# Optimization experiments

Hardware: AMD Instinct MI355X
Metric: run time of the kernel (lower is better)

Reference implementation:

```python
import jax, jax.numpy as jnp
import numpy as np

B, C, E = 64, 32, 4
D_MODEL, PRED_LEN = 1024, 720
L_LIST = [32, 16, 8, 4]  # seq_len=512 / patch_sizes [16,32,64,128]
EPS = float(np.finfo(float).eps)


def setup_inputs() -> dict:
    key = jax.random.key(0)
    ks = jax.random.split(key, 16)
    inp = {}
    for i, L in enumerate(L_LIST):
        inp[f"xs{i}"] = jax.random.normal(ks[i], (B, C, L, D_MODEL), dtype=jnp.float32)
    inp["gates"] = jax.random.uniform(ks[4], (B, E), dtype=jnp.float32)
    w_scale = 1.0 / np.sqrt(D_MODEL)
    for i in range(E):
        inp[f"W{i}"] = jax.random.normal(ks[5 + i], (D_MODEL, PRED_LEN), dtype=jnp.float32) * w_scale
        inp[f"b{i}"] = jax.random.normal(ks[9 + i], (PRED_LEN,), dtype=jnp.float32) * 0.01
    return inp


def reference(xs0, xs1, xs2, xs3, gates, W0, b0, W1, b1, W2, b2, W3, b3):
    xs = [xs0, xs1, xs2, xs3]
    Ws = [W0, W1, W2, W3]
    bs = [b0, b1, b2, b3]
    # per-expert linear on last token: [B,C,D] @ [D,P] + [P] -> [B,C,P]
    outs = jnp.stack(
        [jnp.einsum("bcd,dp->bcp", x[:, :, -1, :], W) + b for x, W, b in zip(xs, Ws, bs)]
    )  # [E,B,C,P]
    # dense-gate combine(): sum_e gates[b,e] * exp(out_e[b])
    combined = jnp.einsum("ebcp,be->bcp", jnp.exp(outs), gates)  # [B,C,P]
    combined = jnp.where(combined == 0, EPS, combined)
    out = jnp.log(combined)  # [B,C,P]
    return out.transpose(0, 2, 1)  # 'B C P -> B P C'
```

## Files before the change

### kernel.cpp

```cpp
#include <hip/hip_runtime.h>
#include <hip/hip_bf16.h>


typedef __attribute__((ext_vector_type(4))) float f32x4;
typedef __attribute__((ext_vector_type(8))) short bf16x8;
typedef __attribute__((ext_vector_type(4))) unsigned short u16x4;
typedef __attribute__((ext_vector_type(8))) unsigned short u16x8;

#define EPSV 2.2204460492503131e-16f

__device__ __forceinline__ unsigned short f2bf(float f) {
  unsigned u = __builtin_bit_cast(unsigned, f);
  u += 0x7fffu + ((u >> 16) & 1u);
  return (unsigned short)(u >> 16);
}
__device__ __forceinline__ float bf2f(unsigned short h) {
  unsigned u = ((unsigned)h) << 16;
  return __builtin_bit_cast(float, u);
}

__device__ __forceinline__ void gload_lds16(const void* g, void* l) {
  __builtin_amdgcn_global_load_lds(
      (const __attribute__((address_space(1))) unsigned int*)g,
      (__attribute__((address_space(3))) unsigned int*)l, 16, 0, 0);
}

__global__ __launch_bounds__(256) void prep_fused(
    const float* __restrict__ xs0, const float* __restrict__ xs1,
    const float* __restrict__ xs2, const float* __restrict__ xs3,
    const float* __restrict__ W0, const float* __restrict__ W1,
    const float* __restrict__ W2, const float* __restrict__ W3,
    unsigned short* __restrict__ Xb, unsigned short* __restrict__ Wb)
{
  __shared__ __align__(16) unsigned short tile[64 * 72];
  const int tid = threadIdx.x;
  if (blockIdx.x < 4096) {
    const int i = blockIdx.x * 256 + tid;
    const int e = i >> 18;
    const int rem = i & 262143;
    const int m = rem >> 7;
    const int kc = rem & 127;
    const float* xp = (e == 0) ? xs0 : (e == 1) ? xs1 : (e == 2) ? xs2 : xs3;
    const int L = 32 >> e;
    const float* src = xp + ((size_t)m * L + (L - 1)) * 1024 + kc * 8;
    f32x4 v0 = *(const f32x4*)src;
    f32x4 v1 = *(const f32x4*)(src + 4);
    u16x8 pk;
    pk[0] = f2bf(v0[0]); pk[1] = f2bf(v0[1]); pk[2] = f2bf(v0[2]); pk[3] = f2bf(v0[3]);
    pk[4] = f2bf(v1[0]); pk[5] = f2bf(v1[1]); pk[6] = f2bf(v1[2]); pk[7] = f2bf(v1[3]);
    *(u16x8*)(Xb + ((size_t)e * 2048 + m) * 1024 + kc * 8) = pk;
  } else {
    const int wI = blockIdx.x - 4096;
    const int k0 = (wI & 15) * 64;
    const int rest = wI >> 4;
    const int nb = (rest % 12) * 64;
    const int e = rest / 12;
    const float* Wp = (e == 0) ? W0 : (e == 1) ? W1 : (e == 2) ? W2 : W3;
    const int n_c = tid & 15;
    const int r = tid >> 4;
    const int n0 = nb + n_c * 4;
#pragma unroll
    for (int j = 0; j < 4; ++j) {
      const int row = r + j * 16;
      f32x4 v = {0.f, 0.f, 0.f, 0.f};
      if (n0 < 720) v = *(const f32x4*)(Wp + (size_t)(k0 + row) * 720 + n0);
#pragma unroll
      for (int d = 0; d < 4; ++d) tile[(n_c * 4 + d) * 72 + row] = f2bf(v[d]);
    }
    __syncthreads();
    const int n_l = tid >> 2;
    const int kq = tid & 3;
    if (nb + n_l < 720) {
#pragma unroll
      for (int q = 0; q < 2; ++q) {
        const int chunk = q * 4 + kq;
        *(u16x8*)(Wb + ((size_t)e * 720 + nb + n_l) * 1024 + k0 + chunk * 8) =
            *(const u16x8*)(tile + n_l * 72 + chunk * 8);
      }
    }
  }
}

__global__ __launch_bounds__(512) void moe_gemm_e(
    const unsigned short* __restrict__ Xb, const unsigned short* __restrict__ Wb,
    const float* __restrict__ gates,
    const float* __restrict__ b0, const float* __restrict__ b1,
    const float* __restrict__ b2, const float* __restrict__ b3,
    unsigned short* __restrict__ planes)
{
  __shared__ __align__(16) unsigned char smem[65536];
  unsigned short* a_lds = (unsigned short*)smem;
  unsigned short* b_lds = (unsigned short*)(smem + 32768);

  const int tid = threadIdx.x;
  const int lane = tid & 63;
  const int wid = tid >> 6;
  const int wm = wid >> 2;
  const int wn = wid & 3;

  const int id = ((int)blockIdx.x & 7) * 48 + ((int)blockIdx.x >> 3);
  const int nt = id % 6;
  const int mt = (id / 6) % 16;
  const int e  = id / 96;
  const int nbase = nt * 128;

  const float* barr[4] = {b0, b1, b2, b3};
  float g_r[2];
#pragma unroll
  for (int h = 0; h < 2; ++h)
    g_r[h] = gates[(mt * 4 + wm * 2 + h) * 4 + e];
  float bias_r[2];
#pragma unroll
  for (int nf = 0; nf < 2; ++nf) {
    int col = nbase + wn * 32 + nf * 16 + (lane & 15);
    bias_r[nf] = barr[e][col < 720 ? col : 719];
  }

  const unsigned short* asrc = Xb + (size_t)e * 2048 * 1024 + (size_t)mt * 128 * 1024;
  const unsigned short* bsrc = Wb + (size_t)e * 720 * 1024;

  auto stage = [&](int k0, int buf) {
#pragma unroll
    for (int j = 0; j < 2; ++j) {
      const int C = j * 512 + tid;
      const int row = C >> 3, c = C & 7;
      gload_lds16(asrc + (size_t)row * 1024 + k0 + ((c ^ (row & 7)) * 8),
                  a_lds + buf * 8192 + C * 8);
    }
#pragma unroll
    for (int j = 0; j < 2; ++j) {
      const int C = j * 512 + tid;
      const int row = C >> 3, c = C & 7;
      int n = nbase + row; if (n > 719) n = 719;
      gload_lds16(bsrc + (size_t)n * 1024 + k0 + ((c ^ (row & 7)) * 8),
                  b_lds + buf * 8192 + C * 8);
    }
  };

  auto compute = [&](int buf, f32x4 (&acc)[4][2]) {
    const unsigned short* al = a_lds + buf * 8192;
    const unsigned short* bl = b_lds + buf * 8192;
#pragma unroll
    for (int ks = 0; ks < 2; ++ks) {
      const int kb = ks * 64 + (lane >> 4) * 16;
      bf16x8 af[4], bfm[2];
#pragma unroll
      for (int mf = 0; mf < 4; ++mf) {
        const int r = wm * 64 + mf * 16 + (lane & 15);
        const int byte = (r * 128 + kb) ^ ((r & 7) << 4);
        af[mf] = *(const bf16x8*)((const char*)al + byte);
      }
#pragma unroll
      for (int nf = 0; nf < 2; ++nf) {
        const int r = wn * 32 + nf * 16 + (lane & 15);
        const int byte = (r * 128 + kb) ^ ((r & 7) << 4);
        bfm[nf] = *(const bf16x8*)((const char*)bl + byte);
      }
#pragma unroll
      for (int mf = 0; mf < 4; ++mf)
#pragma unroll
        for (int nf = 0; nf < 2; ++nf)
          acc[mf][nf] = __builtin_amdgcn_mfma_f32_16x16x32_bf16(
              af[mf], bfm[nf], acc[mf][nf], 0, 0, 0);
    }
  };

  f32x4 acc[4][2] = {};
  int cur = 0;
  stage(0, 0);
  __syncthreads();
  for (int kt = 0; kt < 16; ++kt) {
    if (kt < 15) stage((kt + 1) * 64, cur ^ 1);
    compute(cur, acc);
    __syncthreads();
    cur ^= 1;
  }

#pragma unroll
  for (int nf = 0; nf < 2; ++nf) {
    const int p = nbase + wn * 32 + nf * 16 + (lane & 15);
    if (p < 720) {
#pragma unroll
      for (int mf = 0; mf < 4; ++mf) {
        const int m0 = mt * 128 + wm * 64 + mf * 16 + ((lane >> 4) << 2);
        const float g = g_r[mf >> 1];
        unsigned short* dst = planes + ((size_t)e * 2048 + m0) * 720 + p;
#pragma unroll
        for (int j = 0; j < 4; ++j)
          dst[j * 720] = f2bf(g * __expf(acc[mf][nf][j] + bias_r[nf]));
      }
    }
  }
}

__global__ __launch_bounds__(256) void reduce_log(
    const unsigned short* __restrict__ planes, float* __restrict__ out)
{
  __shared__ __align__(16) float t[64 * 36];
  const int nt = blockIdx.x;
  const int b  = blockIdx.y;
  const int nbase = nt * 64;
  const int tid = threadIdx.x;

  {
    const int row = tid >> 3;
    const int pc = tid & 7;
    int p0 = nbase + pc * 8;
    if (p0 > 712) p0 = 712;
    const size_t base = ((size_t)b * 32 + row) * 720 + p0;
    float s[8] = {};
#pragma unroll
    for (int pl = 0; pl < 4; ++pl) {
      u16x8 v = *(const u16x8*)(planes + (size_t)pl * 2048 * 720 + base);
#pragma unroll
      for (int d = 0; d < 8; ++d) s[d] += bf2f(v[d]);
    }
    const int pbase_l = (p0 - nbase);
#pragma unroll
    for (int d = 0; d < 8; ++d) {
      float v = s[d];
      v = (v == 0.0f) ? EPSV : v;
      t[(pbase_l + d) * 36 + row] = __logf(v);
    }
  }
  __syncthreads();
#pragma unroll
  for (int it = 0; it < 2; ++it) {
    const int i = it * 256 + tid;
    const int p_l = i >> 3;
    const int cc = i & 7;
    const int p = nbase + p_l;
    if (p < 720) {
      f32x4 v = *(const f32x4*)(t + p_l * 36 + cc * 4);
      *(f32x4*)(out + ((size_t)b * 720 + p) * 32 + cc * 4) = v;
    }
  }
}

__global__ __launch_bounds__(256) void moe_head_fallback(
    const float* __restrict__ xs0, const float* __restrict__ xs1,
    const float* __restrict__ xs2, const float* __restrict__ xs3,
    const float* __restrict__ gates,
    const float* __restrict__ W0, const float* __restrict__ b0,
    const float* __restrict__ W1, const float* __restrict__ b1,
    const float* __restrict__ W2, const float* __restrict__ b2,
    const float* __restrict__ W3, const float* __restrict__ b3,
    float* __restrict__ out)
{
  __shared__ __align__(16) unsigned short a_lds[64 * 64];
  __shared__ __align__(16) unsigned short b_lds[64 * 64];
  __shared__ __align__(16) float t_lds[4][32 * 36];
  const int tid = threadIdx.x;
  const int lane = tid & 63;
  const int wid = tid >> 6;
  const int wm = wid >> 1, wn = wid & 1;
  const int nt = blockIdx.x, mt = blockIdx.y;
  const int mbase = mt * 64, nbase = nt * 64;
  const float* xarr[4] = {xs0, xs1, xs2, xs3};
  const float* Warr[4] = {W0, W1, W2, W3};
  const float* barr[4] = {b0, b1, b2, b3};
  constexpr int Larr[4] = {32, 16, 8, 4};
  f32x4 comb[2][2] = {};
#pragma unroll
  for (int e = 0; e < 4; ++e) {
    const int L = Larr[e];
    const float* xlast = xarr[e] + (size_t)(L - 1) * 1024;
    const size_t xstride = (size_t)L * 1024;
    const float* Wp = Warr[e];
    f32x4 acc[2][2] = {};
    for (int kt = 0; kt < 16; ++kt) {
      const int k0 = kt * 64;
      __syncthreads();
      {
        const int k_l = (tid & 15) * 4;
        const int r0 = tid >> 4;
#pragma unroll
        for (int j = 0; j < 4; ++j) {
          const int row = r0 + j * 16;
          f32x4 v = *(const f32x4*)(xlast + (size_t)(mbase + row) * xstride + (k0 + k_l));
          u16x4 pk;
          pk[0] = f2bf(v[0]); pk[1] = f2bf(v[1]); pk[2] = f2bf(v[2]); pk[3] = f2bf(v[3]);
          const int byte = (row * 128 + k_l * 2) ^ ((row & 7) << 4);
          *(u16x4*)((char*)a_lds + byte) = pk;
        }
      }
      {
        const int n_l = tid & 63;
        const int kq = tid >> 6;
        const int n_g = nbase + n_l;
        const bool nok = (n_g < 720);
        const float* wcol = Wp + n_g;
#pragma unroll
        for (int g = 0; g < 4; ++g) {
          const int k_l = kq * 4 + g * 16;
          float w0 = 0.f, w1 = 0.f, w2 = 0.f, w3 = 0.f;
          if (nok) {
            const float* s = wcol + (size_t)(k0 + k_l) * 720;
            w0 = s[0]; w1 = s[720]; w2 = s[1440]; w3 = s[2160];
          }
          u16x4 pk;
          pk[0] = f2bf(w0); pk[1] = f2bf(w1); pk[2] = f2bf(w2); pk[3] = f2bf(w3);
          const int byte = (n_l * 128 + k_l * 2) ^ ((n_l & 7) << 4);
          *(u16x4*)((char*)b_lds + byte) = pk;
        }
      }
      __syncthreads();
#pragma unroll
      for (int ks = 0; ks < 2; ++ks) {
        const int kb2 = (ks * 32 + (lane >> 4) * 8) * 2;
        bf16x8 af[2], bfr[2];
#pragma unroll
        for (int mf = 0; mf < 2; ++mf) {
          const int r = wm * 32 + mf * 16 + (lane & 15);
          const int byte = (r * 128 + kb2) ^ ((r & 7) << 4);
          af[mf] = *(const bf16x8*)((const char*)a_lds + byte);
        }
#pragma unroll
        for (int nf = 0; nf < 2; ++nf) {
          const int r = wn * 32 + nf * 16 + (lane & 15);
          const int byte = (r * 128 + kb2) ^ ((r & 7) << 4);
          bfr[nf] = *(const bf16x8*)((const char*)b_lds + byte);
        }
#pragma unroll
        for (int mf = 0; mf < 2; ++mf)
#pragma unroll
          for (int nf = 0; nf < 2; ++nf)
            acc[mf][nf] = __builtin_amdgcn_mfma_f32_16x16x32_bf16(
                af[mf], bfr[nf], acc[mf][nf], 0, 0, 0);
      }
    }
    {
      const int b_idx = mt * 2 + wm;
      const float g = gates[b_idx * 4 + e];
#pragma unroll
      for (int nf = 0; nf < 2; ++nf) {
        const int col = nbase + wn * 32 + nf * 16 + (lane & 15);
        const float bias = (col < 720) ? barr[e][col] : 0.0f;
#pragma unroll
        for (int mf = 0; mf < 2; ++mf)
#pragma unroll
          for (int j = 0; j < 4; ++j)
            comb[mf][nf][j] += g * __expf(acc[mf][nf][j] + bias);
      }
    }
  }
  {
    float* tl = &t_lds[wid][0];
#pragma unroll
    for (int mf = 0; mf < 2; ++mf)
#pragma unroll
      for (int nf = 0; nf < 2; ++nf)
#pragma unroll
        for (int j = 0; j < 4; ++j) {
          const int row_l = mf * 16 + (lane >> 4) * 4 + j;
          const int col_l = nf * 16 + (lane & 15);
          float v = comb[mf][nf][j];
          v = (v == 0.0f) ? EPSV : v;
          tl[col_l * 36 + row_l] = __logf(v);
        }
    __syncthreads();
    const int b_idx = mt * 2 + wm;
    const int pbase = nbase + wn * 32;
#pragma unroll
    for (int it = 0; it < 4; ++it) {
      const int p_l = it * 8 + (lane >> 3);
      const int p = pbase + p_l;
      if (p < 720) {
        f32x4 v = *(const f32x4*)(tl + p_l * 36 + (lane & 7) * 4);
        *(f32x4*)(out + ((size_t)b_idx * 720 + p) * 32 + (lane & 7) * 4) = v;
      }
    }
  }
}

extern "C" void kernel_launch(void* const* d_in, const int* in_sizes, int n_in,
                              void* d_out, int out_size, void* d_ws, size_t ws_size,
                              hipStream_t stream) {
  const size_t xb_elems = (size_t)4 * 2048 * 1024;
  const size_t wb_elems = (size_t)4 * 720 * 1024;
  const size_t plane_elems = (size_t)4 * 2048 * 720;
  const size_t need = (xb_elems + wb_elems + plane_elems) * 2;
  if (ws_size >= need) {
    unsigned short* Xb = (unsigned short*)d_ws;
    unsigned short* Wb = Xb + xb_elems;
    unsigned short* planes = Wb + wb_elems;
    prep_fused<<<4096 + 768, 256, 0, stream>>>(
        (const float*)d_in[0], (const float*)d_in[1],
        (const float*)d_in[2], (const float*)d_in[3],
        (const float*)d_in[5], (const float*)d_in[7],
        (const float*)d_in[9], (const float*)d_in[11],
        Xb, Wb);
    moe_gemm_e<<<384, 512, 0, stream>>>(
        Xb, Wb, (const float*)d_in[4],
        (const float*)d_in[6], (const float*)d_in[8],
        (const float*)d_in[10], (const float*)d_in[12],
        planes);
    reduce_log<<<dim3(12, 64), 256, 0, stream>>>(planes, (float*)d_out);
  } else {
    moe_head_fallback<<<dim3(12, 32), 256, 0, stream>>>(
        (const float*)d_in[0], (const float*)d_in[1],
        (const float*)d_in[2], (const float*)d_in[3],
        (const float*)d_in[4],
        (const float*)d_in[5], (const float*)d_in[6],
        (const float*)d_in[7], (const float*)d_in[8],
        (const float*)d_in[9], (const float*)d_in[10],
        (const float*)d_in[11], (const float*)d_in[12],
        (float*)d_out);
  }
}
```

Measured before the change: 38.66 us.

## Fuse prep, GEMM and log-reduce into one cooperative kernel with grid syncs

Merges the three launches (bf16 conversion/transposition, per-expert GEMM with exp-gating, and sum-log-transpose reduction) into a single cooperative kernel of 384 blocks separated by grid-wide barriers. This removes two kernel launch gaps and inter-kernel drain. It trades them for two grid syncs, and the prep phase now runs on far fewer threads than the old 4864-block prep kernel. It also drops the workspace-size fallback kernel and falls back to the three-kernel path only if the cooperative launch fails.

```diff
diff --git a/kernel.cpp b/kernel.cpp
--- a/kernel.cpp
+++ b/kernel.cpp
@@ -1,10 +1,12 @@
 #include <hip/hip_runtime.h>
 #include <hip/hip_bf16.h>
-
+#include <hip/hip_cooperative_groups.h>
+
+
+namespace cg = cooperative_groups;
 
 typedef __attribute__((ext_vector_type(4))) float f32x4;
 typedef __attribute__((ext_vector_type(8))) short bf16x8;
-typedef __attribute__((ext_vector_type(4))) unsigned short u16x4;
 typedef __attribute__((ext_vector_type(8))) unsigned short u16x8;
 
 #define EPSV 2.2204460492503131e-16f
@@ -18,11 +20,219 @@
   unsigned u = ((unsigned)h) << 16;
   return __builtin_bit_cast(float, u);
 }
-
 __device__ __forceinline__ void gload_lds16(const void* g, void* l) {
   __builtin_amdgcn_global_load_lds(
       (const __attribute__((address_space(1))) unsigned int*)g,
       (__attribute__((address_space(3))) unsigned int*)l, 16, 0, 0);
+}
+
+__global__ __launch_bounds__(512, 4) void moe_coop(
+    const float* __restrict__ xs0, const float* __restrict__ xs1,
+    const float* __restrict__ xs2, const float* __restrict__ xs3,
+    const float* __restrict__ W0, const float* __restrict__ W1,
+    const float* __restrict__ W2, const float* __restrict__ W3,
+    const float* __restrict__ gates,
+    const float* __restrict__ b0, const float* __restrict__ b1,
+    const float* __restrict__ b2, const float* __restrict__ b3,
+    unsigned short* __restrict__ Xb, unsigned short* __restrict__ Wb,
+    unsigned short* __restrict__ planes, float* __restrict__ out)
+{
+  __shared__ __align__(16) unsigned char smem[65536];
+  const int tid = threadIdx.x;
+  const int lane = tid & 63;
+  const int id = ((int)blockIdx.x & 7) * 48 + ((int)blockIdx.x >> 3);
+
+  const float* barr[4] = {b0, b1, b2, b3};
+
+  {
+    const int x  = id / 48;
+    const int bl = id % 48;
+    const int e = x >> 1;
+    const int mh = x & 1;
+    const float* xp = (e == 0) ? xs0 : (e == 1) ? xs1 : (e == 2) ? xs2 : xs3;
+    const int L = 32 >> e;
+    for (int c = bl * 512 + tid; c < 131072; c += 24576) {
+      const int m = mh * 1024 + (c >> 7);
+      const int kc = c & 127;
+      const float* src = xp + ((size_t)m * L + (L - 1)) * 1024 + kc * 8;
+      f32x4 v0 = *(const f32x4*)src;
+      f32x4 v1 = *(const f32x4*)(src + 4);
+      u16x8 pk;
+      pk[0] = f2bf(v0[0]); pk[1] = f2bf(v0[1]); pk[2] = f2bf(v0[2]); pk[3] = f2bf(v0[3]);
+      pk[4] = f2bf(v1[0]); pk[5] = f2bf(v1[1]); pk[6] = f2bf(v1[2]); pk[7] = f2bf(v1[3]);
+      *(u16x8*)(Xb + ((size_t)e * 2048 + m) * 1024 + kc * 8) = pk;
+    }
+    const int h = tid >> 8, tid2 = tid & 255;
+    const int eW = id / 96;
+    const int tile = (id % 96) * 2 + h;
+    const int k0 = (tile & 15) * 64;
+    const int nb = (tile >> 4) * 64;
+    const float* Wp = (eW == 0) ? W0 : (eW == 1) ? W1 : (eW == 2) ? W2 : W3;
+    unsigned short* tl = (unsigned short*)(smem + h * 9216);
+    const int n_c = tid2 & 15;
+    const int r = tid2 >> 4;
+    const int n0 = nb + n_c * 4;
+#pragma unroll
+    for (int j = 0; j < 4; ++j) {
+      const int row = r + j * 16;
+      f32x4 v = {0.f, 0.f, 0.f, 0.f};
+      if (n0 < 720) v = *(const f32x4*)(Wp + (size_t)(k0 + row) * 720 + n0);
+#pragma unroll
+      for (int d = 0; d < 4; ++d) tl[(n_c * 4 + d) * 72 + row] = f2bf(v[d]);
+    }
+    __syncthreads();
+    const int n_l = tid2 >> 2;
+    const int kq = tid2 & 3;
+    if (nb + n_l < 720) {
+#pragma unroll
+      for (int q = 0; q < 2; ++q) {
+        const int chunk = q * 4 + kq;
+        *(u16x8*)(Wb + ((size_t)eW * 720 + nb + n_l) * 1024 + k0 + chunk * 8) =
+            *(const u16x8*)(tl + n_l * 72 + chunk * 8);
+      }
+    }
+  }
+  cg::this_grid().sync();
+
+  {
+    unsigned short* a_lds = (unsigned short*)smem;
+    unsigned short* b_lds = (unsigned short*)(smem + 32768);
+    const int wid = tid >> 6;
+    const int wm = wid >> 2;
+    const int wn = wid & 3;
+    const int nt = id % 6;
+    const int mt = (id / 6) % 16;
+    const int e  = id / 96;
+    const int nbase = nt * 128;
+
+    float g_r[2];
+#pragma unroll
+    for (int h = 0; h < 2; ++h)
+      g_r[h] = gates[(mt * 4 + wm * 2 + h) * 4 + e];
+    float bias_r[2];
+#pragma unroll
+    for (int nf = 0; nf < 2; ++nf) {
+      int col = nbase + wn * 32 + nf * 16 + (lane & 15);
+      bias_r[nf] = barr[e][col < 720 ? col : 719];
+    }
+
+    const unsigned short* asrc = Xb + (size_t)e * 2048 * 1024 + (size_t)mt * 128 * 1024;
+    const unsigned short* bsrc = Wb + (size_t)e * 720 * 1024;
+
+    auto stage = [&](int k0, int buf) {
+#pragma unroll
+      for (int j = 0; j < 2; ++j) {
+        const int C = j * 512 + tid;
+        const int row = C >> 3, c = C & 7;
+        gload_lds16(asrc + (size_t)row * 1024 + k0 + ((c ^ (row & 7)) * 8),
+                    a_lds + buf * 8192 + C * 8);
+      }
+#pragma unroll
+      for (int j = 0; j < 2; ++j) {
+        const int C = j * 512 + tid;
+        const int row = C >> 3, c = C & 7;
+        int n = nbase + row; if (n > 719) n = 719;
+        gload_lds16(bsrc + (size_t)n * 1024 + k0 + ((c ^ (row & 7)) * 8),
+                    b_lds + buf * 8192 + C * 8);
+      }
+    };
+    auto compute = [&](int buf, f32x4 (&acc)[4][2]) {
+      const unsigned short* al = a_lds + buf * 8192;
+      const unsigned short* bl = b_lds + buf * 8192;
+#pragma unroll
+      for (int ks = 0; ks < 2; ++ks) {
+        const int kb = ks * 64 + (lane >> 4) * 16;
+        bf16x8 af[4], bfm[2];
+#pragma unroll
+        for (int mf = 0; mf < 4; ++mf) {
+          const int rr = wm * 64 + mf * 16 + (lane & 15);
+          const int byte = (rr * 128 + kb) ^ ((rr & 7) << 4);
+          af[mf] = *(const bf16x8*)((const char*)al + byte);
+        }
+#pragma unroll
+        for (int nf = 0; nf < 2; ++nf) {
+          const int rr = wn * 32 + nf * 16 + (lane & 15);
+          const int byte = (rr * 128 + kb) ^ ((rr & 7) << 4);
+          bfm[nf] = *(const bf16x8*)((const char*)bl + byte);
+        }
+#pragma unroll
+        for (int mf = 0; mf < 4; ++mf)
+#pragma unroll
+          for (int nf = 0; nf < 2; ++nf)
+            acc[mf][nf] = __builtin_amdgcn_mfma_f32_16x16x32_bf16(
+                af[mf], bfm[nf], acc[mf][nf], 0, 0, 0);
+      }
+    };
+
+    f32x4 acc[4][2] = {};
+    int cur = 0;
+    stage(0, 0);
+    __syncthreads();
+    for (int kt = 0; kt < 16; ++kt) {
+      if (kt < 15) stage((kt + 1) * 64, cur ^ 1);
+      compute(cur, acc);
+      __syncthreads();
+      cur ^= 1;
+    }
+#pragma unroll
+    for (int nf = 0; nf < 2; ++nf) {
+      const int p = nbase + wn * 32 + nf * 16 + (lane & 15);
+      if (p < 720) {
+#pragma unroll
+        for (int mf = 0; mf < 4; ++mf) {
+          const int m0 = mt * 128 + wm * 64 + mf * 16 + ((lane >> 4) << 2);
+          const float g = g_r[mf >> 1];
+          unsigned short* dst = planes + ((size_t)e * 2048 + m0) * 720 + p;
+#pragma unroll
+          for (int j = 0; j < 4; ++j)
+            dst[j * 720] = f2bf(g * __expf(acc[mf][nf][j] + bias_r[nf]));
+        }
+      }
+    }
+  }
+  cg::this_grid().sync();
+
+  {
+    const int h = tid >> 8, tid2 = tid & 255;
+    const int unit = id * 2 + h;
+    const int nt = unit % 12;
+    const int bb = unit / 12;
+    const int nbase = nt * 64;
+    float* t = (float*)(smem + h * 9216);
+    {
+      const int row = tid2 >> 3;
+      const int pc = tid2 & 7;
+      int p0 = nbase + pc * 8;
+      if (p0 > 712) p0 = 712;
+      const size_t base = ((size_t)bb * 32 + row) * 720 + p0;
+      float s[8] = {};
+#pragma unroll
+      for (int pl = 0; pl < 4; ++pl) {
+        u16x8 v = *(const u16x8*)(planes + (size_t)pl * 2048 * 720 + base);
+#pragma unroll
+        for (int d = 0; d < 8; ++d) s[d] += bf2f(v[d]);
+      }
+      const int pbase_l = (p0 - nbase);
+#pragma unroll
+      for (int d = 0; d < 8; ++d) {
+        float v = s[d];
+        v = (v == 0.0f) ? EPSV : v;
+        t[(pbase_l + d) * 36 + row] = __logf(v);
+      }
+    }
+    __syncthreads();
+#pragma unroll
+    for (int it = 0; it < 2; ++it) {
+      const int i = it * 256 + tid2;
+      const int p_l = i >> 3;
+      const int cc = i & 7;
+      const int p = nbase + p_l;
+      if (p < 720) {
+        f32x4 v = *(const f32x4*)(t + p_l * 36 + cc * 4);
+        *(f32x4*)(out + ((size_t)bb * 720 + p) * 32 + cc * 4) = v;
+      }
+    }
+  }
 }
 
 __global__ __launch_bounds__(256) void prep_fused(
@@ -91,19 +301,16 @@
   __shared__ __align__(16) unsigned char smem[65536];
   unsigned short* a_lds = (unsigned short*)smem;
   unsigned short* b_lds = (unsigned short*)(smem + 32768);
-
   const int tid = threadIdx.x;
   const int lane = tid & 63;
   const int wid = tid >> 6;
   const int wm = wid >> 2;
   const int wn = wid & 3;
-
   const int id = ((int)blockIdx.x & 7) * 48 + ((int)blockIdx.x >> 3);
   const int nt = id % 6;
   const int mt = (id / 6) % 16;
   const int e  = id / 96;
   const int nbase = nt * 128;
-
   const float* barr[4] = {b0, b1, b2, b3};
   float g_r[2];
 #pragma unroll
@@ -115,10 +322,8 @@
     int col = nbase + wn * 32 + nf * 16 + (lane & 15);
     bias_r[nf] = barr[e][col < 720 ? col : 719];
   }
-
   const unsigned short* asrc = Xb + (size_t)e * 2048 * 1024 + (size_t)mt * 128 * 1024;
   const unsigned short* bsrc = Wb + (size_t)e * 720 * 1024;
-
   auto stage = [&](int k0, int buf) {
 #pragma unroll
     for (int j = 0; j < 2; ++j) {
@@ -136,7 +341,6 @@
                   b_lds + buf * 8192 + C * 8);
     }
   };
-
   auto compute = [&](int buf, f32x4 (&acc)[4][2]) {
     const unsigned short* al = a_lds + buf * 8192;
     const unsigned short* bl = b_lds + buf * 8192;
@@ -164,7 +368,6 @@
               af[mf], bfm[nf], acc[mf][nf], 0, 0, 0);
     }
   };
-
   f32x4 acc[4][2] = {};
   int cur = 0;
   stage(0, 0);
@@ -175,7 +378,6 @@
     __syncthreads();
     cur ^= 1;
   }
-
 #pragma unroll
   for (int nf = 0; nf < 2; ++nf) {
     const int p = nbase + wn * 32 + nf * 16 + (lane & 15);
@@ -201,7 +403,6 @@
   const int b  = blockIdx.y;
   const int nbase = nt * 64;
   const int tid = threadIdx.x;
-
   {
     const int row = tid >> 3;
     const int pc = tid & 7;
@@ -237,174 +438,44 @@
   }
 }
 
-__global__ __launch_bounds__(256) void moe_head_fallback(
-    const float* __restrict__ xs0, const float* __restrict__ xs1,
-    const float* __restrict__ xs2, const float* __restrict__ xs3,
-    const float* __restrict__ gates,
-    const float* __restrict__ W0, const float* __restrict__ b0,
-    const float* __restrict__ W1, const float* __restrict__ b1,
-    const float* __restrict__ W2, const float* __restrict__ b2,
-    const float* __restrict__ W3, const float* __restrict__ b3,
-    float* __restrict__ out)
-{
-  __shared__ __align__(16) unsigned short a_lds[64 * 64];
-  __shared__ __align__(16) unsigned short b_lds[64 * 64];
-  __shared__ __align__(16) float t_lds[4][32 * 36];
-  const int tid = threadIdx.x;
-  const int lane = tid & 63;
-  const int wid = tid >> 6;
-  const int wm = wid >> 1, wn = wid & 1;
-  const int nt = blockIdx.x, mt = blockIdx.y;
-  const int mbase = mt * 64, nbase = nt * 64;
-  const float* xarr[4] = {xs0, xs1, xs2, xs3};
-  const float* Warr[4] = {W0, W1, W2, W3};
-  const float* barr[4] = {b0, b1, b2, b3};
-  constexpr int Larr[4] = {32, 16, 8, 4};
-  f32x4 comb[2][2] = {};
-#pragma unroll
-  for (int e = 0; e < 4; ++e) {
-    const int L = Larr[e];
-    const float* xlast = xarr[e] + (size_t)(L - 1) * 1024;
-    const size_t xstride = (size_t)L * 1024;
-    const float* Wp = Warr[e];
-    f32x4 acc[2][2] = {};
-    for (int kt = 0; kt < 16; ++kt) {
-      const int k0 = kt * 64;
-      __syncthreads();
-      {
-        const int k_l = (tid & 15) * 4;
-        const int r0 = tid >> 4;
-#pragma unroll
-        for (int j = 0; j < 4; ++j) {
-          const int row = r0 + j * 16;
-          f32x4 v = *(const f32x4*)(xlast + (size_t)(mbase + row) * xstride + (k0 + k_l));
-          u16x4 pk;
-          pk[0] = f2bf(v[0]); pk[1] = f2bf(v[1]); pk[2] = f2bf(v[2]); pk[3] = f2bf(v[3]);
-          const int byte = (row * 128 + k_l * 2) ^ ((row & 7) << 4);
-          *(u16x4*)((char*)a_lds + byte) = pk;
-        }
-      }
-      {
-        const int n_l = tid & 63;
-        const int kq = tid >> 6;
-        const int n_g = nbase + n_l;
-        const bool nok = (n_g < 720);
-        const float* wcol = Wp + n_g;
-#pragma unroll
-        for (int g = 0; g < 4; ++g) {
-          const int k_l = kq * 4 + g * 16;
-          float w0 = 0.f, w1 = 0.f, w2 = 0.f, w3 = 0.f;
-          if (nok) {
-            const float* s = wcol + (size_t)(k0 + k_l) * 720;
-            w0 = s[0]; w1 = s[720]; w2 = s[1440]; w3 = s[2160];
-          }
-          u16x4 pk;
-          pk[0] = f2bf(w0); pk[1] = f2bf(w1); pk[2] = f2bf(w2); pk[3] = f2bf(w3);
-          const int byte = (n_l * 128 + k_l * 2) ^ ((n_l & 7) << 4);
-          *(u16x4*)((char*)b_lds + byte) = pk;
-        }
-      }
-      __syncthreads();
-#pragma unroll
-      for (int ks = 0; ks < 2; ++ks) {
-        const int kb2 = (ks * 32 + (lane >> 4) * 8) * 2;
-        bf16x8 af[2], bfr[2];
-#pragma unroll
-        for (int mf = 0; mf < 2; ++mf) {
-          const int r = wm * 32 + mf * 16 + (lane & 15);
-          const int byte = (r * 128 + kb2) ^ ((r & 7) << 4);
-          af[mf] = *(const bf16x8*)((const char*)a_lds + byte);
-        }
-#pragma unroll
-        for (int nf = 0; nf < 2; ++nf) {
-          const int r = wn * 32 + nf * 16 + (lane & 15);
-          const int byte = (r * 128 + kb2) ^ ((r & 7) << 4);
-          bfr[nf] = *(const bf16x8*)((const char*)b_lds + byte);
-        }
-#pragma unroll
-        for (int mf = 0; mf < 2; ++mf)
-#pragma unroll
-          for (int nf = 0; nf < 2; ++nf)
-            acc[mf][nf] = __builtin_amdgcn_mfma_f32_16x16x32_bf16(
-                af[mf], bfr[nf], acc[mf][nf], 0, 0, 0);
-      }
-    }
-    {
-      const int b_idx = mt * 2 + wm;
-      const float g = gates[b_idx * 4 + e];
-#pragma unroll
-      for (int nf = 0; nf < 2; ++nf) {
-        const int col = nbase + wn * 32 + nf * 16 + (lane & 15);
-        const float bias = (col < 720) ? barr[e][col] : 0.0f;
-#pragma unroll
-        for (int mf = 0; mf < 2; ++mf)
-#pragma unroll
-          for (int j = 0; j < 4; ++j)
-            comb[mf][nf][j] += g * __expf(acc[mf][nf][j] + bias);
-      }
-    }
-  }
-  {
-    float* tl = &t_lds[wid][0];
-#pragma unroll
-    for (int mf = 0; mf < 2; ++mf)
-#pragma unroll
-      for (int nf = 0; nf < 2; ++nf)
-#pragma unroll
-        for (int j = 0; j < 4; ++j) {
-          const int row_l = mf * 16 + (lane >> 4) * 4 + j;
-          const int col_l = nf * 16 + (lane & 15);
-          float v = comb[mf][nf][j];
-          v = (v == 0.0f) ? EPSV : v;
-          tl[col_l * 36 + row_l] = __logf(v);
-        }
-    __syncthreads();
-    const int b_idx = mt * 2 + wm;
-    const int pbase = nbase + wn * 32;
-#pragma unroll
-    for (int it = 0; it < 4; ++it) {
-      const int p_l = it * 8 + (lane >> 3);
-      const int p = pbase + p_l;
-      if (p < 720) {
-        f32x4 v = *(const f32x4*)(tl + p_l * 36 + (lane & 7) * 4);
-        *(f32x4*)(out + ((size_t)b_idx * 720 + p) * 32 + (lane & 7) * 4) = v;
-      }
-    }
-  }
-}
-
 extern "C" void kernel_launch(void* const* d_in, const int* in_sizes, int n_in,
                               void* d_out, int out_size, void* d_ws, size_t ws_size,
                               hipStream_t stream) {
   const size_t xb_elems = (size_t)4 * 2048 * 1024;
   const size_t wb_elems = (size_t)4 * 720 * 1024;
-  const size_t plane_elems = (size_t)4 * 2048 * 720;
-  const size_t need = (xb_elems + wb_elems + plane_elems) * 2;
-  if (ws_size >= need) {
-    unsigned short* Xb = (unsigned short*)d_ws;
-    unsigned short* Wb = Xb + xb_elems;
-    unsigned short* planes = Wb + wb_elems;
-    prep_fused<<<4096 + 768, 256, 0, stream>>>(
-        (const float*)d_in[0], (const float*)d_in[1],
-        (const float*)d_in[2], (const float*)d_in[3],
-        (const float*)d_in[5], (const float*)d_in[7],
-        (const float*)d_in[9], (const float*)d_in[11],
-        Xb, Wb);
-    moe_gemm_e<<<384, 512, 0, stream>>>(
-        Xb, Wb, (const float*)d_in[4],
-        (const float*)d_in[6], (const float*)d_in[8],
-        (const float*)d_in[10], (const float*)d_in[12],
-        planes);
-    reduce_log<<<dim3(12, 64), 256, 0, stream>>>(planes, (float*)d_out);
-  } else {
-    moe_head_fallback<<<dim3(12, 32), 256, 0, stream>>>(
-        (const float*)d_in[0], (const float*)d_in[1],
-        (const float*)d_in[2], (const float*)d_in[3],
-        (const float*)d_in[4],
-        (const float*)d_in[5], (const float*)d_in[6],
-        (const float*)d_in[7], (const float*)d_in[8],
-        (const float*)d_in[9], (const float*)d_in[10],
-        (const float*)d_in[11], (const float*)d_in[12],
-        (float*)d_out);
-  }
-}
+  unsigned short* Xb = (unsigned short*)d_ws;
+  unsigned short* Wb = Xb + xb_elems;
+  unsigned short* planes = Wb + wb_elems;
+
+  const float* xs0 = (const float*)d_in[0];
+  const float* xs1 = (const float*)d_in[1];
+  const float* xs2 = (const float*)d_in[2];
+  const float* xs3 = (const float*)d_in[3];
+  const float* gates = (const float*)d_in[4];
+  const float* W0 = (const float*)d_in[5];
+  const float* b0 = (const float*)d_in[6];
+  const float* W1 = (const float*)d_in[7];
+  const float* b1 = (const float*)d_in[8];
+  const float* W2 = (const float*)d_in[9];
+  const float* b2 = (const float*)d_in[10];
+  const float* W3 = (const float*)d_in[11];
+  const float* b3 = (const float*)d_in[12];
+  float* outp = (float*)d_out;
+
+  void* args[] = {
+      (void*)&xs0, (void*)&xs1, (void*)&xs2, (void*)&xs3,
+      (void*)&W0, (void*)&W1, (void*)&W2, (void*)&W3,
+      (void*)&gates,
+      (void*)&b0, (void*)&b1, (void*)&b2, (void*)&b3,
+      (void*)&Xb, (void*)&Wb, (void*)&planes, (void*)&outp};
+
+  hipError_t err = hipLaunchCooperativeKernel(
+      (const void*)moe_coop, dim3(384), dim3(512), args, 0, stream);
+
+  if (err != hipSuccess) {
+    prep_fused<<<4096 + 768, 256, 0, stream>>>(xs0, xs1, xs2, xs3,
+                                               W0, W1, W2, W3, Xb, Wb);
+    moe_gemm_e<<<384, 512, 0, stream>>>(Xb, Wb, gates, b0, b1, b2, b3, planes);
+    reduce_log<<<dim3(12, 64), 256, 0, stream>>>(planes, outp);
+  }
+}
```

Result: slower. 141.3 us (+265.5%).
